# Kernel optimization log

Measured on AMD Instinct MI355X. Metric: run time of the kernel, lower is better.

Reference implementation:

```python
import jax, jax.numpy as jnp
import numpy as np

B, T, DIM = 2, 2048, 2048
H, HKV = 16, 4
D = DIM // H          # head_dim = 128
G = H // HKV          # GQA group = 4
ROPE_BASE = 10000.0
TRAIN_SEQ_LEN = 1024  # Rotary default; T > this triggers NTK base rescale


def _rope_tables():
    # Faithful to Rotary.forward: NTK scaling when seq_len > train_seq_len.
    if T > TRAIN_SEQ_LEN:
        sc = T / TRAIN_SEQ_LEN
        base = ROPE_BASE * sc ** (D / (D - 2))
    else:
        base = ROPE_BASE
    inv = 1.0 / base ** (np.arange(0, D, 2, dtype=np.float32) / D)  # [D/2]
    f = np.outer(np.arange(T, dtype=np.float32), inv)               # [T, D/2]
    cos = jnp.asarray(np.cos(f), jnp.float32)[None, :, None, :]     # [1,T,1,D/2]
    sin = jnp.asarray(np.sin(f), jnp.float32)[None, :, None, :]
    return cos, sin


def _rms_norm(x):
    # F.rms_norm with no weight: x / sqrt(mean(x^2) + eps), eps = finfo(dtype).eps
    eps = jnp.finfo(x.dtype).eps
    return x * jax.lax.rsqrt(jnp.mean(x * x, axis=-1, keepdims=True) + eps)


def _apply_rope(x, cos, sin):
    x1, x2 = jnp.split(x, 2, axis=-1)
    return jnp.concatenate([x1 * cos + x2 * sin, -x1 * sin + x2 * cos], axis=-1)


def setup_inputs() -> dict:
    key = jax.random.key(0)
    kx, kq, kk, kv, kp = jax.random.split(key, 5)
    s = lambda fan_in: 1.0 / np.sqrt(fan_in)
    kv_dim = HKV * D
    return {
        "x": jax.random.normal(kx, (B, T, DIM), jnp.float32),
        "Wq": jax.random.normal(kq, (DIM, DIM), jnp.float32) * s(DIM),
        "Wk": jax.random.normal(kk, (kv_dim, DIM), jnp.float32) * s(DIM),
        "Wv": jax.random.normal(kv, (kv_dim, DIM), jnp.float32) * s(DIM),
        "Wproj": jax.random.normal(kp, (DIM, DIM), jnp.float32) * s(DIM),
        "q_gain": jnp.full((H,), 1.0, jnp.float32),
    }


def reference(x, Wq, Wk, Wv, Wproj, q_gain):
    # QKV projections (bias-free linears)
    q = (x @ Wq.T).reshape(B, T, H, D)
    k = (x @ Wk.T).reshape(B, T, HKV, D)
    v = (x @ Wv.T).reshape(B, T, HKV, D)

    # QK RMSNorm + RoPE + per-head q gain
    q = _rms_norm(q)
    k = _rms_norm(k)
    cos, sin = _rope_tables()
    q = _apply_rope(q, cos, sin)
    k = _apply_rope(k, cos, sin)
    q = q * q_gain[None, None, :, None]

    # GQA causal SDPA without materializing repeated K/V:
    # group query heads by kv head: q -> [B,T,HKV,G,D]
    qg = q.reshape(B, T, HKV, G, D)
    scores = jnp.einsum('btkgd,bskd->bkgts', qg, k) / np.sqrt(D)  # [B,HKV,G,T,T]
    causal = jnp.tril(jnp.ones((T, T), bool))
    scores = jnp.where(causal[None, None, None], scores, -jnp.inf)
    p = jax.nn.softmax(scores, axis=-1)
    y = jnp.einsum('bkgts,bskd->btkgd', p, v).reshape(B, T, H, D)

    out = y.reshape(B, T, DIM) @ Wproj.T
    return out, v
```

## Files before the change

kernel.cpp:

```cpp
#include <hip/hip_runtime.h>
#include <hip/hip_bf16.h>

typedef __bf16 bf16_t;
typedef __bf16 bf16x4 __attribute__((ext_vector_type(4)));
typedef __bf16 bf16x8 __attribute__((ext_vector_type(8)));
typedef float f32x4 __attribute__((ext_vector_type(4)));

#define B_    2
#define T_    2048
#define DIM_  2048
#define H_    16
#define HKV_  4
#define D_    128
#define KVDIM_ 512

__device__ __forceinline__ bf16x8 cvt8(f32x4 a, f32x4 b) {
  bf16x8 r;
  r[0] = (bf16_t)a[0]; r[1] = (bf16_t)a[1]; r[2] = (bf16_t)a[2]; r[3] = (bf16_t)a[3];
  r[4] = (bf16_t)b[0]; r[5] = (bf16_t)b[1]; r[6] = (bf16_t)b[2]; r[7] = (bf16_t)b[3];
  return r;
}
__device__ __forceinline__ bf16x4 cvt4(f32x4 a) {
  bf16x4 r;
  r[0] = (bf16_t)a[0]; r[1] = (bf16_t)a[1]; r[2] = (bf16_t)a[2]; r[3] = (bf16_t)a[3];
  return r;
}
__device__ __forceinline__ void g2l16(const void* g, void* l) {
  __builtin_amdgcn_global_load_lds(
      (const __attribute__((address_space(1))) unsigned int*)g,
      (__attribute__((address_space(3))) unsigned int*)l, 16, 0, 0);
}

__global__ __launch_bounds__(256)
void cvt_all(const float* __restrict__ x,  const float* __restrict__ wq,
             const float* __restrict__ wk, const float* __restrict__ wv,
             const float* __restrict__ wp, bf16_t* __restrict__ xb,
             bf16_t* __restrict__ wqkvb, bf16_t* __restrict__ wpb) {
  int blk = blockIdx.x;
  const float* s; bf16_t* d; int lb;
  if (blk < 4096)      { s = x;  d = xb;                              lb = blk; }
  else if (blk < 6144) { s = wq; d = wqkvb;                           lb = blk - 4096; }
  else if (blk < 6656) { s = wk; d = wqkvb + (size_t)2048 * DIM_;     lb = blk - 6144; }
  else if (blk < 7168) { s = wv; d = wqkvb + (size_t)2560 * DIM_;     lb = blk - 6656; }
  else                 { s = wp; d = wpb;                             lb = blk - 7168; }
  size_t i = (size_t)lb * 2048 + (size_t)threadIdx.x * 8;
  f32x4 a = *(const f32x4*)(s + i);
  f32x4 b = *(const f32x4*)(s + i + 4);
  *(bf16x8*)(d + i) = cvt8(a, b);
}

template <int MODE, bool AASYNC, bool WASYNC>
__global__ __launch_bounds__(256)
void gemm128(const void* __restrict__ Ag, const void* __restrict__ Wg,
             const void* __restrict__ Wg2, void* __restrict__ Cb,
             bf16_t* __restrict__ Kb, bf16_t* __restrict__ Vb,
             float* __restrict__ Vf, int M, int N, int K) {
  constexpr int LDA = AASYNC ? 32 : 40;
  constexpr int LDW = WASYNC ? 32 : 40;
  __shared__ bf16_t As[128 * LDA];
  __shared__ bf16_t Ws[128 * LDW];
  const int tid  = threadIdx.x;
  const int wave = tid >> 6, lane = tid & 63;
  const int l16  = lane & 15, lg = lane >> 4;
  const int m0 = blockIdx.y * 128, n0 = blockIdx.x * 128;
  const int wm = (wave & 1) * 64, wn = (wave >> 1) * 64;
  f32x4 acc[4][4] = {};

  for (int k0 = 0; k0 < K; k0 += 32) {
    __syncthreads();
    if constexpr (AASYNC) {
      const bf16_t* A = (const bf16_t*)Ag;
      const int r = lane >> 2, c8 = (lane & 3) * 8;
      g2l16(&A[(size_t)(m0 + wave * 32 + r) * K + k0 + c8],      &As[(wave * 32) * LDA]);
      g2l16(&A[(size_t)(m0 + wave * 32 + 16 + r) * K + k0 + c8], &As[(wave * 32 + 16) * LDA]);
    } else {
      const float* A = (const float*)Ag;
#pragma unroll
      for (int j = 0; j < 4; j++) {
        int row = wave * 32 + j * 8 + (lane >> 3);
        int cf  = (lane & 7) * 4;
        f32x4 v = *(const f32x4*)&A[(size_t)(m0 + row) * K + k0 + cf];
        *(bf16x4*)&As[row * LDA + cf] = cvt4(v);
      }
    }
    if constexpr (WASYNC) {
      const bf16_t* W = (const bf16_t*)Wg;
      const int r = lane >> 2, c8 = (lane & 3) * 8;
      g2l16(&W[(size_t)(n0 + wave * 32 + r) * K + k0 + c8],      &Ws[(wave * 32) * LDW]);
      g2l16(&W[(size_t)(n0 + wave * 32 + 16 + r) * K + k0 + c8], &Ws[(wave * 32 + 16) * LDW]);
    } else {
      const float* W;
      int nb;
      if constexpr (MODE == 3) {
        if (n0 < 512) { W = (const float*)Wg;  nb = n0; }
        else          { W = (const float*)Wg2; nb = n0 - 512; }
      } else { W = (const float*)Wg; nb = n0; }
#pragma unroll
      for (int j = 0; j < 4; j++) {
        int row = wave * 32 + j * 8 + (lane >> 3);
        int cf  = (lane & 7) * 4;
        f32x4 v = *(const f32x4*)&W[(size_t)(nb + row) * K + k0 + cf];
        *(bf16x4*)&Ws[row * LDW + cf] = cvt4(v);
      }
    }
    __syncthreads();
    bf16x8 af[4], bfr[4];
#pragma unroll
    for (int i = 0; i < 4; i++)
      af[i] = *(const bf16x8*)&As[(wm + i * 16 + l16) * LDA + lg * 8];
#pragma unroll
    for (int j = 0; j < 4; j++)
      bfr[j] = *(const bf16x8*)&Ws[(wn + j * 16 + l16) * LDW + lg * 8];
#pragma unroll
    for (int i = 0; i < 4; i++)
#pragma unroll
      for (int j = 0; j < 4; j++)
        acc[i][j] = __builtin_amdgcn_mfma_f32_16x16x32_bf16(af[i], bfr[j], acc[i][j], 0, 0, 0);
  }
#pragma unroll
  for (int i = 0; i < 4; i++)
#pragma unroll
    for (int j = 0; j < 4; j++) {
      int row = m0 + wm + i * 16 + lg * 4;
      int col = n0 + wn + j * 16 + l16;
#pragma unroll
      for (int r = 0; r < 4; r++) {
        float v = acc[i][j][r];
        if constexpr (MODE == 0) {
          ((bf16_t*)Cb)[(size_t)(row + r) * N + col] = (bf16_t)v;
        } else if constexpr (MODE == 2) {
          ((float*)Cb)[(size_t)(row + r) * N + col] = v;
        } else if constexpr (MODE == 1) {
          if (col < 2048)      ((bf16_t*)Cb)[(size_t)(row + r) * 2048 + col] = (bf16_t)v;
          else if (col < 2560) Kb[(size_t)(row + r) * 512 + (col - 2048)] = (bf16_t)v;
          else {
            int c = col - 2560;
            Vb[(size_t)(row + r) * 512 + c] = (bf16_t)v;
            Vf[(size_t)(row + r) * 512 + c] = v;
          }
        } else {
          if (col < 512) ((bf16_t*)Cb)[(size_t)(row + r) * 512 + col] = (bf16_t)v;
          else {
            int c = col - 512;
            Vb[(size_t)(row + r) * 512 + c] = (bf16_t)v;
            Vf[(size_t)(row + r) * 512 + c] = v;
          }
        }
      }
    }
}

#define SB() __builtin_amdgcn_sched_barrier(0)
#define BARRIER() __builtin_amdgcn_s_barrier()
#define LGKM0() do { asm volatile("s_waitcnt lgkmcnt(0)" ::: "memory"); SB(); } while (0)
#define VMW(N) do { asm volatile("s_waitcnt vmcnt(" #N ")" ::: "memory"); SB(); } while (0)

#define RD_A(BUF, QM) do { \
  _Pragma("unroll") for (int f_ = 0; f_ < 4; f_++) { \
    const int r_ = wm * 128 + (QM) * 64 + f_ * 16 + l16; \
    _Pragma("unroll") for (int ks_ = 0; ks_ < 2; ks_++) \
      a[f_][ks_] = *(const bf16x8*)(lds + (BUF) * 65536 + r_ * 128 + ((ks_ * 64 + lg * 16) ^ swz)); \
  } } while (0)

#define RD_B(BUF, QN, BB) do { \
  _Pragma("unroll") for (int n_ = 0; n_ < 2; n_++) { \
    const int r_ = wn * 64 + (QN) * 32 + n_ * 16 + l16; \
    _Pragma("unroll") for (int ks_ = 0; ks_ < 2; ks_++) \
      BB[n_][ks_] = *(const bf16x8*)(lds + (BUF) * 65536 + 32768 + r_ * 128 + ((ks_ * 64 + lg * 16) ^ swz)); \
  } } while (0)

#define MM(QM, QN, BB) do { \
  __builtin_amdgcn_s_setprio(1); \
  _Pragma("unroll") for (int f_ = 0; f_ < 4; f_++) \
    _Pragma("unroll") for (int n_ = 0; n_ < 2; n_++) \
      _Pragma("unroll") for (int ks_ = 0; ks_ < 2; ks_++) \
        acc[(QM) * 4 + f_][(QN) * 2 + n_] = __builtin_amdgcn_mfma_f32_16x16x32_bf16( \
            a[f_][ks_], BB[n_][ks_], acc[(QM) * 4 + f_][(QN) * 2 + n_], 0, 0, 0); \
  __builtin_amdgcn_s_setprio(0); \
  } while (0)

#define K_ITER(KT0, LAST) do { \
  const int kA1_ = ((KT0) + 1) * 64; \
  const int kN2_ = ((KT0) + 2) * 64; \
  const int kN3_ = ((KT0) + 3) * 64; \
   \
  RD_A(0, 0); RD_B(0, 0, b0); \
  stage_half(Ag, m0, kA1_, 65536); \
  asm volatile("s_waitcnt lgkmcnt(8)" ::: "memory"); \
  SB(); BARRIER(); LGKM0(); \
  MM(0, 0, b0); \
  SB(); BARRIER(); \
   \
  RD_B(0, 1, b1); \
  stage_half(Ag, m0 + 128, kA1_, 65536 + 16384); \
  SB(); BARRIER(); LGKM0(); \
  MM(0, 1, b1); \
  SB(); BARRIER(); \
   \
  RD_A(0, 1); \
  if (!(LAST)) stage_half(Wg, n0, kN2_, 32768); \
  SB(); BARRIER(); LGKM0(); \
  MM(1, 0, b0); \
  SB(); BARRIER(); \
   \
  if (!(LAST)) { stage_half(Wg, n0 + 128, kN2_, 32768 + 16384); VMW(4); } \
  else { VMW(0); } \
  SB(); BARRIER(); \
  MM(1, 1, b1); \
  SB(); BARRIER(); \
   \
  RD_A(1, 0); RD_B(1, 0, b0); \
  if (!(LAST)) stage_half(Ag, m0, kN2_, 0); \
  asm volatile("s_waitcnt lgkmcnt(8)" ::: "memory"); \
  SB(); BARRIER(); LGKM0(); \
  MM(0, 0, b0); \
  SB(); BARRIER(); \
   \
  RD_B(1, 1, b1); \
  if (!(LAST)) stage_half(Ag, m0 + 128, kN2_, 16384); \
  SB(); BARRIER(); LGKM0(); \
  MM(0, 1, b1); \
  SB(); BARRIER(); \
   \
  RD_A(1, 1); \
  if (!(LAST)) stage_half(Wg, n0, kN3_, 65536 + 32768); \
  SB(); BARRIER(); LGKM0(); \
  MM(1, 0, b0); \
  SB(); BARRIER(); \
   \
  if (!(LAST)) { stage_half(Wg, n0 + 128, kN3_, 65536 + 32768 + 16384); VMW(4); } \
  SB(); BARRIER(); \
  MM(1, 1, b1); \
  SB(); BARRIER(); \
} while (0)

template <int MODE>
__global__ __launch_bounds__(512, 2)
void gemm256(const bf16_t* __restrict__ Ag, const bf16_t* __restrict__ Wg,
             void* __restrict__ Cb, bf16_t* __restrict__ Kb, bf16_t* __restrict__ Vb,
             float* __restrict__ Vf, int M, int N, int K) {
  (void)M;
  __shared__ __align__(16) char lds[131072];
  const int tid  = threadIdx.x;
  const int wave = tid >> 6, lane = tid & 63;
  const int l16  = lane & 15, lg = lane >> 4;
  const int wm = wave >> 2, wn = wave & 3;
  const int swz = (l16 & 7) << 4;
  const int m0 = blockIdx.y * 256, n0 = blockIdx.x * 256;
  const int srow = lane >> 3;
  const int scol = ((lane & 7) ^ srow) * 8;

  auto stage_half = [&](const bf16_t* __restrict__ X, int xrow, int k0, int ldsoff) {
    const bf16_t* src = X + (size_t)(xrow + wave * 16 + srow) * K + (k0 + scol);
    char* dst = lds + ldsoff + wave * 2048;
    g2l16(src, dst);
    g2l16(src + (size_t)8 * K, dst + 1024);
  };

  f32x4 acc[8][4] = {};
  bf16x8 a[4][2], b0[2][2], b1[2][2];

  stage_half(Ag, m0,        0, 0);
  stage_half(Ag, m0 + 128,  0, 16384);
  stage_half(Wg, n0,        0, 32768);
  stage_half(Wg, n0 + 128,  0, 32768 + 16384);
  stage_half(Wg, n0,       64, 65536 + 32768);
  stage_half(Wg, n0 + 128, 64, 65536 + 32768 + 16384);
  VMW(4);
  BARRIER();

  const int NIT = K >> 7;
  for (int it = 0; it < NIT - 1; ++it) {
    K_ITER(2 * it, 0);
  }
  K_ITER(2 * (NIT - 1), 1);

#pragma unroll
  for (int mf = 0; mf < 8; mf++)
#pragma unroll
    for (int nf = 0; nf < 4; nf++) {
      const int row = m0 + wm * 128 + mf * 16 + lg * 4;
      const int col = n0 + wn * 64 + nf * 16 + l16;
#pragma unroll
      for (int r = 0; r < 4; r++) {
        float v = acc[mf][nf][r];
        if constexpr (MODE == 1) {
          if (col < 2048)      ((bf16_t*)Cb)[(size_t)(row + r) * 2048 + col] = (bf16_t)v;
          else if (col < 2560) Kb[(size_t)(row + r) * 512 + (col - 2048)] = (bf16_t)v;
          else {
            int c = col - 2560;
            Vb[(size_t)(row + r) * 512 + c] = (bf16_t)v;
            Vf[(size_t)(row + r) * 512 + c] = v;
          }
        } else {
          ((float*)Cb)[(size_t)(row + r) * N + col] = v;
        }
      }
    }
}

__global__ __launch_bounds__(256)
void qk_norm_rope(bf16_t* __restrict__ Qp, bf16_t* __restrict__ Kp,
                  const float* __restrict__ gain) {
  const int lane = threadIdx.x & 63;
  int row = blockIdx.x * 4 + (threadIdx.x >> 6);
  bf16_t* Xp; int nh; bool ag;
  const int MQ = B_ * T_ * H_;
  if (row < MQ) { Xp = Qp; nh = H_;  ag = true; }
  else          { Xp = Kp; nh = HKV_; ag = false; row -= MQ; }
  const int h = row % nh;
  const int t = (row / nh) % T_;
  bf16_t* p = Xp + (size_t)row * D_;
  float x0 = (float)p[lane * 2 + 0];
  float x1 = (float)p[lane * 2 + 1];
  float ss = x0 * x0 + x1 * x1;
#pragma unroll
  for (int m = 32; m >= 1; m >>= 1) ss += __shfl_xor(ss, m);
  const float rn = rsqrtf(ss * (1.0f / 128.0f) + 1.1920929e-07f);
  x0 *= rn; x1 *= rn;
  const float y0 = __shfl_xor(x0, 32);
  const float y1 = __shfl_xor(x1, 32);
  const int i0 = (lane & 31) * 2;
  const float kfreq = -0.22349352180347601f;
  float s0, c0, s1, c1;
  float a0 = (float)t * exp2f(kfreq * (float)i0);
  float a1 = (float)t * exp2f(kfreq * (float)(i0 + 1));
  sincosf(a0, &s0, &c0);
  sincosf(a1, &s1, &c1);
  float o0, o1;
  if (lane < 32) { o0 = x0 * c0 + y0 * s0;  o1 = x1 * c1 + y1 * s1; }
  else           { o0 = x0 * c0 - y0 * s0;  o1 = x1 * c1 - y1 * s1; }
  if (ag) { float g = gain[h]; o0 *= g; o1 *= g; }
  p[lane * 2 + 0] = (bf16_t)o0;
  p[lane * 2 + 1] = (bf16_t)o1;
}

#define KLD 136
#define VLD 72
#define PLD 68

__global__ __launch_bounds__(256, 2)
void flash_attn(const bf16_t* __restrict__ Q, const bf16_t* __restrict__ Kg,
                const bf16_t* __restrict__ V, bf16_t* __restrict__ Y) {
  __shared__ bf16_t Ks[64 * KLD];
  __shared__ bf16_t Vs[D_ * VLD];
  __shared__ float  Ps[4][16 * PLD];
  const int tid  = threadIdx.x;
  const int wave = tid >> 6, lane = tid & 63;
  const int l16  = lane & 15, lg = lane >> 4;
  const int b = blockIdx.z, h = blockIdx.y;
  const int pi = blockIdx.x;
  const int hk = h >> 2;

  int qr[2];
  qr[0] = 64 * pi + 16 * wave;
  qr[1] = 64 * (31 - pi) + 16 * wave;

  bf16x8 qf[2][4];
#pragma unroll
  for (int mt = 0; mt < 2; mt++)
#pragma unroll
    for (int kk = 0; kk < 4; kk++)
      qf[mt][kk] = *(const bf16x8*)&Q[(((size_t)b * T_ + qr[mt] + l16) * H_ + h) * D_ + kk * 32 + lg * 8];

  f32x4 o[2][8] = {};
  float lsum[2][4] = {};
  const float C = 0.12752531f;

  const int sr = tid >> 4, sc = (tid & 15) * 8;
  const int sp2 = (tid & 31) * 2;
  const int dvh = (tid >> 5) * 8;

  bf16x8 kreg[4];
  bf16x8 vreg[2][2];
  auto pf_load = [&](int k0) {
#pragma unroll
    for (int j = 0; j < 4; j++)
      kreg[j] = *(const bf16x8*)&Kg[(((size_t)b * T_ + k0 + sr + 16 * j) * HKV_ + hk) * D_ + sc];
#pragma unroll
    for (int it = 0; it < 2; it++) {
      const bf16_t* vb = &V[(((size_t)b * T_ + k0 + sp2) * HKV_ + hk) * D_ + dvh + it * 64];
      vreg[it][0] = *(const bf16x8*)vb;
      vreg[it][1] = *(const bf16x8*)(vb + HKV_ * D_);
    }
  };
  auto pf_store = [&]() {
#pragma unroll
    for (int j = 0; j < 4; j++)
      *(bf16x8*)&Ks[(sr + 16 * j) * KLD + sc] = kreg[j];
#pragma unroll
    for (int it = 0; it < 2; it++) {
      int dd = dvh + it * 64;
      const unsigned short* au = (const unsigned short*)&vreg[it][0];
      const unsigned short* bu = (const unsigned short*)&vreg[it][1];
#pragma unroll
      for (int i = 0; i < 8; i++) {
        unsigned int pr = (unsigned int)au[i] | ((unsigned int)bu[i] << 16);
        *(unsigned int*)&Vs[(dd + i) * VLD + sp2] = pr;
      }
    }
  };

  const int nkb = 32 - pi;
  pf_load(0);
  for (int kb = 0; kb < nkb; kb++) {
    const int k0 = kb * 64;
    __syncthreads();
    pf_store();
    __syncthreads();
    if (kb + 1 < nkb) pf_load(k0 + 64);

    const bool act0 = (kb <= pi);

    f32x4 s[2][4] = {};
#pragma unroll
    for (int kk = 0; kk < 4; kk++) {
      bf16x8 kf[4];
#pragma unroll
      for (int f = 0; f < 4; f++)
        kf[f] = *(const bf16x8*)&Ks[(f * 16 + l16) * KLD + kk * 32 + lg * 8];
      if (act0)
#pragma unroll
        for (int f = 0; f < 4; f++)
          s[0][f] = __builtin_amdgcn_mfma_f32_16x16x32_bf16(qf[0][kk], kf[f], s[0][f], 0, 0, 0);
#pragma unroll
      for (int f = 0; f < 4; f++)
        s[1][f] = __builtin_amdgcn_mfma_f32_16x16x32_bf16(qf[1][kk], kf[f], s[1][f], 0, 0, 0);
    }
    bf16x8 pf[2][2];
    float* pw = Ps[wave];
#pragma unroll
    for (int mt = 0; mt < 2; mt++) {
      if (mt == 0 && !act0) continue;
      const bool diag = (mt == 0) ? (kb == pi) : (kb == nkb - 1);
      if (diag) {
        const int myq = qr[mt] + lg * 4;
#pragma unroll
        for (int f = 0; f < 4; f++)
#pragma unroll
          for (int r = 0; r < 4; r++) {
            int kcol = k0 + f * 16 + l16;
            float p = (kcol <= myq + r) ? exp2f(s[mt][f][r] * C) : 0.0f;
            lsum[mt][r] += p;
            pw[(lg * 4 + r) * PLD + f * 16 + l16] = p;
          }
      } else {
#pragma unroll
        for (int f = 0; f < 4; f++)
#pragma unroll
          for (int r = 0; r < 4; r++) {
            float p = exp2f(s[mt][f][r] * C);
            lsum[mt][r] += p;
            pw[(lg * 4 + r) * PLD + f * 16 + l16] = p;
          }
      }
      __threadfence_block();
      f32x4 pa0 = *(const f32x4*)&pw[l16 * PLD + lg * 8];
      f32x4 pa1 = *(const f32x4*)&pw[l16 * PLD + lg * 8 + 4];
      f32x4 pb0 = *(const f32x4*)&pw[l16 * PLD + 32 + lg * 8];
      f32x4 pb1 = *(const f32x4*)&pw[l16 * PLD + 32 + lg * 8 + 4];
      pf[mt][0] = cvt8(pa0, pa1);
      pf[mt][1] = cvt8(pb0, pb1);
      __threadfence_block();
    }
#pragma unroll
    for (int f = 0; f < 8; f++) {
      bf16x8 v0 = *(const bf16x8*)&Vs[(f * 16 + l16) * VLD + lg * 8];
      bf16x8 v1 = *(const bf16x8*)&Vs[(f * 16 + l16) * VLD + 32 + lg * 8];
      if (act0) {
        o[0][f] = __builtin_amdgcn_mfma_f32_16x16x32_bf16(pf[0][0], v0, o[0][f], 0, 0, 0);
        o[0][f] = __builtin_amdgcn_mfma_f32_16x16x32_bf16(pf[0][1], v1, o[0][f], 0, 0, 0);
      }
      o[1][f] = __builtin_amdgcn_mfma_f32_16x16x32_bf16(pf[1][0], v0, o[1][f], 0, 0, 0);
      o[1][f] = __builtin_amdgcn_mfma_f32_16x16x32_bf16(pf[1][1], v1, o[1][f], 0, 0, 0);
    }
  }
#pragma unroll
  for (int mt = 0; mt < 2; mt++) {
    float rl[4];
#pragma unroll
    for (int r = 0; r < 4; r++) {
      float l = lsum[mt][r];
      l += __shfl_xor(l, 1);
      l += __shfl_xor(l, 2);
      l += __shfl_xor(l, 4);
      l += __shfl_xor(l, 8);
      rl[r] = 1.0f / l;
    }
#pragma unroll
    for (int f = 0; f < 8; f++)
#pragma unroll
      for (int r = 0; r < 4; r++) {
        int t = qr[mt] + lg * 4 + r;
        Y[(((size_t)b * T_ + t) * H_ + h) * D_ + f * 16 + l16] = (bf16_t)(o[mt][f][r] * rl[r]);
      }
  }
}

extern "C" void kernel_launch(void* const* d_in, const int* in_sizes, int n_in,
                              void* d_out, int out_size, void* d_ws, size_t ws_size,
                              hipStream_t stream) {
  (void)in_sizes; (void)n_in; (void)out_size;
  const float* x     = (const float*)d_in[0];
  const float* Wq    = (const float*)d_in[1];
  const float* Wk    = (const float*)d_in[2];
  const float* Wv    = (const float*)d_in[3];
  const float* Wproj = (const float*)d_in[4];
  const float* qgain = (const float*)d_in[5];

  float* out  = (float*)d_out;
  float* vout = out + (size_t)B_ * T_ * DIM_;

  const size_t M = (size_t)B_ * T_;
  char* ws = (char*)d_ws;
  size_t off = 0;
  auto take = [&](size_t elems) { bf16_t* p = (bf16_t*)(ws + off); off += elems * sizeof(bf16_t); return p; };

  bf16_t* Qp = take(M * DIM_);
  bf16_t* Kp = take(M * KVDIM_);
  bf16_t* Vb = take(M * KVDIM_);

  const size_t cvt_elems = M * DIM_ + (size_t)3072 * DIM_ + (size_t)DIM_ * DIM_;
  const bool fast = (ws_size >= off + cvt_elems * sizeof(bf16_t));

  dim3 blk(256);
  if (fast) {
    bf16_t* xb     = take(M * DIM_);
    bf16_t* Wqkvb  = take((size_t)3072 * DIM_);
    bf16_t* Wpb    = take((size_t)DIM_ * DIM_);

    cvt_all<<<dim3(9216), blk, 0, stream>>>(x, Wq, Wk, Wv, Wproj, xb, Wqkvb, Wpb);

    gemm256<1><<<dim3(3072 / 256, M / 256), dim3(512), 0, stream>>>(
        xb, Wqkvb, Qp, Kp, Vb, vout, (int)M, 3072, DIM_);

    qk_norm_rope<<<dim3((unsigned)((M * H_ + M * HKV_) / 4)), blk, 0, stream>>>(Qp, Kp, qgain);
    flash_attn<<<dim3(16, H_, B_), blk, 0, stream>>>(Qp, Kp, Vb, Qp);

    gemm256<2><<<dim3(DIM_ / 256, M / 256), dim3(512), 0, stream>>>(
        Qp, Wpb, out, nullptr, nullptr, nullptr, (int)M, DIM_, DIM_);
  } else {
    gemm128<0, false, false><<<dim3(DIM_ / 128, M / 128), blk, 0, stream>>>(
        x, Wq, nullptr, Qp, nullptr, nullptr, nullptr, M, DIM_, DIM_);
    gemm128<3, false, false><<<dim3(2 * KVDIM_ / 128, M / 128), blk, 0, stream>>>(
        x, Wk, Wv, Kp, nullptr, Vb, vout, M, 2 * KVDIM_, DIM_);
    qk_norm_rope<<<dim3((unsigned)((M * H_ + M * HKV_) / 4)), blk, 0, stream>>>(Qp, Kp, qgain);
    flash_attn<<<dim3(16, H_, B_), blk, 0, stream>>>(Qp, Kp, Vb, Qp);
    gemm128<2, true, false><<<dim3(DIM_ / 128, M / 128), blk, 0, stream>>>(
        Qp, Wproj, nullptr, out, nullptr, nullptr, nullptr, M, DIM_, DIM_);
  }
}
```

Before: 317.6 us.

## Compute transposed S=K·Qᵀ so P stays in registers, permute V layout

```diff
diff --git a/kernel.cpp b/kernel.cpp
--- a/kernel.cpp
+++ b/kernel.cpp
@@ -337,14 +337,12 @@
 
 #define KLD 136
 #define VLD 72
-#define PLD 68
 
 __global__ __launch_bounds__(256, 2)
 void flash_attn(const bf16_t* __restrict__ Q, const bf16_t* __restrict__ Kg,
                 const bf16_t* __restrict__ V, bf16_t* __restrict__ Y) {
   __shared__ bf16_t Ks[64 * KLD];
   __shared__ bf16_t Vs[D_ * VLD];
-  __shared__ float  Ps[4][16 * PLD];
   const int tid  = threadIdx.x;
   const int wave = tid >> 6, lane = tid & 63;
   const int l16  = lane & 15, lg = lane >> 4;
@@ -364,12 +362,14 @@
       qf[mt][kk] = *(const bf16x8*)&Q[(((size_t)b * T_ + qr[mt] + l16) * H_ + h) * D_ + kk * 32 + lg * 8];
 
   f32x4 o[2][8] = {};
-  float lsum[2][4] = {};
+  float lsum[2] = {};
   const float C = 0.12752531f;
 
   const int sr = tid >> 4, sc = (tid & 15) * 8;
   const int sp2 = (tid & 31) * 2;
   const int dvh = (tid >> 5) * 8;
+  const int ssl = (sp2 & 3) | (((sp2 >> 4) & 1) << 2) | (((sp2 >> 2) & 1) << 3)
+                | (((sp2 >> 3) & 1) << 4) | (sp2 & 32);
 
   bf16x8 kreg[4];
   bf16x8 vreg[2][2];
@@ -396,7 +396,7 @@
 #pragma unroll
       for (int i = 0; i < 8; i++) {
         unsigned int pr = (unsigned int)au[i] | ((unsigned int)bu[i] << 16);
-        *(unsigned int*)&Vs[(dd + i) * VLD + sp2] = pr;
+        *(unsigned int*)&Vs[(dd + i) * VLD + ssl] = pr;
       }
     }
   };
@@ -422,27 +422,26 @@
       if (act0)
 #pragma unroll
         for (int f = 0; f < 4; f++)
-          s[0][f] = __builtin_amdgcn_mfma_f32_16x16x32_bf16(qf[0][kk], kf[f], s[0][f], 0, 0, 0);
+          s[0][f] = __builtin_amdgcn_mfma_f32_16x16x32_bf16(kf[f], qf[0][kk], s[0][f], 0, 0, 0);
 #pragma unroll
       for (int f = 0; f < 4; f++)
-        s[1][f] = __builtin_amdgcn_mfma_f32_16x16x32_bf16(qf[1][kk], kf[f], s[1][f], 0, 0, 0);
-    }
-    bf16x8 pf[2][2];
-    float* pw = Ps[wave];
+        s[1][f] = __builtin_amdgcn_mfma_f32_16x16x32_bf16(kf[f], qf[1][kk], s[1][f], 0, 0, 0);
+    }
+    bf16x8 pfr[2][2];
 #pragma unroll
     for (int mt = 0; mt < 2; mt++) {
       if (mt == 0 && !act0) continue;
       const bool diag = (mt == 0) ? (kb == pi) : (kb == nkb - 1);
+      const int myq = qr[mt] + l16;
       if (diag) {
-        const int myq = qr[mt] + lg * 4;
 #pragma unroll
         for (int f = 0; f < 4; f++)
 #pragma unroll
           for (int r = 0; r < 4; r++) {
-            int kcol = k0 + f * 16 + l16;
-            float p = (kcol <= myq + r) ? exp2f(s[mt][f][r] * C) : 0.0f;
-            lsum[mt][r] += p;
-            pw[(lg * 4 + r) * PLD + f * 16 + l16] = p;
+            int kg = k0 + f * 16 + lg * 4 + r;
+            float p = (kg <= myq) ? exp2f(s[mt][f][r] * C) : 0.0f;
+            lsum[mt] += p;
+            s[mt][f][r] = p;
           }
       } else {
 #pragma unroll
@@ -450,49 +449,40 @@
 #pragma unroll
           for (int r = 0; r < 4; r++) {
             float p = exp2f(s[mt][f][r] * C);
-            lsum[mt][r] += p;
-            pw[(lg * 4 + r) * PLD + f * 16 + l16] = p;
+            lsum[mt] += p;
+            s[mt][f][r] = p;
           }
       }
-      __threadfence_block();
-      f32x4 pa0 = *(const f32x4*)&pw[l16 * PLD + lg * 8];
-      f32x4 pa1 = *(const f32x4*)&pw[l16 * PLD + lg * 8 + 4];
-      f32x4 pb0 = *(const f32x4*)&pw[l16 * PLD + 32 + lg * 8];
-      f32x4 pb1 = *(const f32x4*)&pw[l16 * PLD + 32 + lg * 8 + 4];
-      pf[mt][0] = cvt8(pa0, pa1);
-      pf[mt][1] = cvt8(pb0, pb1);
-      __threadfence_block();
+      pfr[mt][0] = cvt8(s[mt][0], s[mt][1]);
+      pfr[mt][1] = cvt8(s[mt][2], s[mt][3]);
     }
 #pragma unroll
     for (int f = 0; f < 8; f++) {
       bf16x8 v0 = *(const bf16x8*)&Vs[(f * 16 + l16) * VLD + lg * 8];
       bf16x8 v1 = *(const bf16x8*)&Vs[(f * 16 + l16) * VLD + 32 + lg * 8];
       if (act0) {
-        o[0][f] = __builtin_amdgcn_mfma_f32_16x16x32_bf16(pf[0][0], v0, o[0][f], 0, 0, 0);
-        o[0][f] = __builtin_amdgcn_mfma_f32_16x16x32_bf16(pf[0][1], v1, o[0][f], 0, 0, 0);
-      }
-      o[1][f] = __builtin_amdgcn_mfma_f32_16x16x32_bf16(pf[1][0], v0, o[1][f], 0, 0, 0);
-      o[1][f] = __builtin_amdgcn_mfma_f32_16x16x32_bf16(pf[1][1], v1, o[1][f], 0, 0, 0);
+        o[0][f] = __builtin_amdgcn_mfma_f32_16x16x32_bf16(pfr[0][0], v0, o[0][f], 0, 0, 0);
+        o[0][f] = __builtin_amdgcn_mfma_f32_16x16x32_bf16(pfr[0][1], v1, o[0][f], 0, 0, 0);
+      }
+      o[1][f] = __builtin_amdgcn_mfma_f32_16x16x32_bf16(pfr[1][0], v0, o[1][f], 0, 0, 0);
+      o[1][f] = __builtin_amdgcn_mfma_f32_16x16x32_bf16(pfr[1][1], v1, o[1][f], 0, 0, 0);
     }
   }
 #pragma unroll
   for (int mt = 0; mt < 2; mt++) {
-    float rl[4];
-#pragma unroll
-    for (int r = 0; r < 4; r++) {
-      float l = lsum[mt][r];
-      l += __shfl_xor(l, 1);
-      l += __shfl_xor(l, 2);
-      l += __shfl_xor(l, 4);
-      l += __shfl_xor(l, 8);
-      rl[r] = 1.0f / l;
-    }
+    float l = lsum[mt];
+    l += __shfl_xor(l, 16);
+    l += __shfl_xor(l, 32);
+    const float inv = 1.0f / l;
+    float rlv[4];
+#pragma unroll
+    for (int r = 0; r < 4; r++) rlv[r] = __shfl(inv, lg * 4 + r);
 #pragma unroll
     for (int f = 0; f < 8; f++)
 #pragma unroll
       for (int r = 0; r < 4; r++) {
         int t = qr[mt] + lg * 4 + r;
-        Y[(((size_t)b * T_ + t) * H_ + h) * D_ + f * 16 + l16] = (bf16_t)(o[mt][f][r] * rl[r]);
+        Y[(((size_t)b * T_ + t) * H_ + h) * D_ + f * 16 + l16] = (bf16_t)(o[mt][f][r] * rlv[r]);
       }
   }
 }
```

After: 315.0 us. Within noise of the previous version (-0.8%).
